# Kernel tuning notes

Hardware: AMD Instinct MI355X
Metric: run time of the kernel (lower is better)

Reference implementation:

```python
import jax, jax.numpy as jnp
import numpy as np

N = 100000      # n_nodes
E = 1600000     # n_edges (avg degree 16)
D_IN, D_H, D_OUT = 128, 64, 16


def setup_inputs() -> dict:
    key = jax.random.key(0)
    k1, k2, k3, k4 = jax.random.split(key, 4)
    x = jax.random.normal(k1, (N, D_IN), dtype=jnp.float32)
    edge_index = jax.random.randint(k2, (2, E), 0, N, dtype=jnp.int32)
    W1 = jax.random.normal(k3, (D_IN, D_H), dtype=jnp.float32) / np.sqrt(D_IN)
    b1 = jnp.zeros((D_H,), dtype=jnp.float32)
    W2 = jax.random.normal(k4, (D_H, D_OUT), dtype=jnp.float32) / np.sqrt(D_H)
    b2 = jnp.zeros((D_OUT,), dtype=jnp.float32)
    return {"x": x, "edge_index": edge_index, "W1": W1, "b1": b1, "W2": W2, "b2": b2}


def gcn_conv(x, src, dst, W, b, n):
    """PyG GCNConv: linear transform, then deg^-1/2 A deg^-1/2 aggregation, + bias.
    src/dst already include self-loops."""
    h = x @ W                                              # [n, d_out]
    deg = jax.ops.segment_sum(jnp.ones_like(dst, dtype=h.dtype), dst, num_segments=n)
    dinv = jnp.where(deg > 0, jax.lax.rsqrt(jnp.maximum(deg, 1.0)), 0.0)
    norm = dinv[src] * dinv[dst]                           # [E+n]
    msgs = h[src] * norm[:, None]                          # gather + scale
    out = jax.ops.segment_sum(msgs, dst, num_segments=n)   # scatter-add
    return out + b


def reference(x, edge_index, W1, b1, W2, b2):
    loops = jnp.arange(N, dtype=edge_index.dtype)
    src = jnp.concatenate([edge_index[0], loops])
    dst = jnp.concatenate([edge_index[1], loops])
    h = jax.nn.relu(gcn_conv(x, src, dst, W1, b1, N))
    return gcn_conv(h, src, dst, W2, b2, N)
```

## Files before the change

kernel.cpp:

```cpp
#include <hip/hip_runtime.h>
#include <cstdint>

#define N_NODES 100000
#define N_EDGES 1600000
#define D_IN    128
#define D_H     64
#define D_OUT   16
#define M_TILES 6250

#define NBKT   512
#define NPB    196
#define BCAP   4096
#define TILE_E 4096
#define NTILES ((N_EDGES + TILE_E - 1) / TILE_E)
#define G1     391
#define GEMM_BLOCKS ((M_TILES + 3) / 4)
#define FUSED_LDS 32768

typedef __attribute__((ext_vector_type(8))) short short8;
typedef __attribute__((ext_vector_type(4))) float floatx4;

static __device__ __forceinline__ unsigned short f2bf(float f) {
    unsigned int u = __float_as_uint(f);
    u = u + 0x7FFFu + ((u >> 16) & 1u);
    return (unsigned short)(u >> 16);
}
static __device__ __forceinline__ float bf2f(unsigned short h) {
    return __uint_as_float(((unsigned int)h) << 16);
}


__global__ __launch_bounds__(512) void zero_small_kernel(int* __restrict__ cursors,
                                                         int* __restrict__ srcs) {
    cursors[threadIdx.x] = 0;
    if (threadIdx.x < 16) srcs[N_EDGES + threadIdx.x] = 0;
}

__global__ __launch_bounds__(256) void fused_bin_gemm1_kernel(
        const int* __restrict__ src, const int* __restrict__ dst,
        int* __restrict__ cursors, int* __restrict__ region,
        const float* __restrict__ x, const float* __restrict__ W1,
        float* __restrict__ h_raw) {
    extern __shared__ char smem[];
    const int t = threadIdx.x;

    if (blockIdx.x < G1) {
        int* hcnt  = (int*)smem;
        int* hbase = (int*)(smem + 2048);
        const int tile = blockIdx.x;
        for (int i = t; i < NBKT; i += 256) hcnt[i] = 0;
        __syncthreads();
        int e0 = tile * TILE_E + t * 16;
        int pk[16], bk[16], rk[16];
        bool full = (e0 + 16 <= N_EDGES);
        if (full) {
            const int4* dp = (const int4*)(dst + e0);
            const int4* sp = (const int4*)(src + e0);
            int dv[16], sv[16];
            #pragma unroll
            for (int q = 0; q < 4; ++q) {
                int4 d4 = dp[q]; int4 s4 = sp[q];
                dv[4*q+0]=d4.x; dv[4*q+1]=d4.y; dv[4*q+2]=d4.z; dv[4*q+3]=d4.w;
                sv[4*q+0]=s4.x; sv[4*q+1]=s4.y; sv[4*q+2]=s4.z; sv[4*q+3]=s4.w;
            }
            #pragma unroll
            for (int k = 0; k < 16; ++k) {
                int d = dv[k];
                int b = d / NPB;
                bk[k] = b;
                pk[k] = ((d - b * NPB) << 17) | sv[k];
                rk[k] = atomicAdd(&hcnt[b], 1);
            }
        }
        __syncthreads();
        for (int i = t; i < NBKT; i += 256) {
            int c = hcnt[i];
            if (c > 0) hbase[i] = atomicAdd(&cursors[i], c);
        }
        __syncthreads();
        if (full) {
            #pragma unroll
            for (int k = 0; k < 16; ++k)
                region[bk[k] * BCAP + hbase[bk[k]] + rk[k]] = pk[k];
        }
        return;
    }

    unsigned short* bhi_lds = (unsigned short*)smem;
    unsigned short* blo_lds = (unsigned short*)(smem + 16384);
    for (int e = t; e < 8192; e += 256) {
        int j    = e & 7;
        int lane = (e >> 3) & 63;
        int pair = e >> 9;
        int kc   = pair >> 2;
        int nt   = pair & 3;
        int k = kc * 32 + (lane >> 4) * 8 + j;
        int n = nt * 16 + (lane & 15);
        float w = W1[k * D_H + n];
        unsigned short hi = f2bf(w);
        float lo = w - bf2f(hi);
        bhi_lds[e] = hi;
        blo_lds[e] = f2bf(lo);
    }
    __syncthreads();

    int wid  = t >> 6;
    int lane = t & 63;
    int quad = lane >> 4;
    int m    = lane & 15;

    int tile = (blockIdx.x - G1) * 4 + wid;
    if (tile >= M_TILES) return;
    int mbase = tile * 16;

    const float* xr = x + (size_t)(mbase + m) * D_IN + quad * 8;
    short8 ahi[4], alo[4];
    #pragma unroll
    for (int kc = 0; kc < 4; ++kc) {
        floatx4 v0 = *(const floatx4*)(xr + kc * 32);
        floatx4 v1 = *(const floatx4*)(xr + kc * 32 + 4);
        float f[8] = {v0.x, v0.y, v0.z, v0.w, v1.x, v1.y, v1.z, v1.w};
        #pragma unroll
        for (int j = 0; j < 8; ++j) {
            unsigned short hi = f2bf(f[j]);
            float lo = f[j] - bf2f(hi);
            ahi[kc][j] = (short)hi;
            alo[kc][j] = (short)f2bf(lo);
        }
    }

    floatx4 acc[4] = {{0.f,0.f,0.f,0.f},{0.f,0.f,0.f,0.f},{0.f,0.f,0.f,0.f},{0.f,0.f,0.f,0.f}};
    #pragma unroll
    for (int kc = 0; kc < 4; ++kc) {
        #pragma unroll
        for (int nt = 0; nt < 4; ++nt) {
            int fo = ((kc * 4 + nt) * 64 + lane) * 8;
            short8 bhi = *(const short8*)&bhi_lds[fo];
            short8 blo = *(const short8*)&blo_lds[fo];
            acc[nt] = __builtin_amdgcn_mfma_f32_16x16x32_bf16(ahi[kc], bhi, acc[nt], 0, 0, 0);
            acc[nt] = __builtin_amdgcn_mfma_f32_16x16x32_bf16(ahi[kc], blo, acc[nt], 0, 0, 0);
            acc[nt] = __builtin_amdgcn_mfma_f32_16x16x32_bf16(alo[kc], bhi, acc[nt], 0, 0, 0);
        }
    }

    #pragma unroll
    for (int nt = 0; nt < 4; ++nt) {
        int col = nt * 16 + m;
        #pragma unroll
        for (int r = 0; r < 4; ++r) {
            int row = mbase + quad * 4 + r;
            h_raw[(size_t)row * D_H + col] = acc[nt][r];
        }
    }
}

__global__ __launch_bounds__(256) void build_kernel(const int* __restrict__ cursors,
                                                    const int* __restrict__ region,
                                                    int* __restrict__ offsets,
                                                    float* __restrict__ dinv,
                                                    int* __restrict__ srcs,
                                                    const float* __restrict__ h_raw,
                                                    unsigned short* __restrict__ hs) {
    __shared__ int lhist[NPB];
    __shared__ int lscan[NPB + 1];
    __shared__ int sbuf[256];
    __shared__ int srt[BCAP];
    __shared__ int red[4];
    __shared__ float sdv[NPB];
    int b = blockIdx.x;
    int t = threadIdx.x;

    int c0 = cursors[t];
    int c1 = cursors[t + 256];
    int p = ((t < b) ? c0 : 0) + ((t + 256 < b) ? c1 : 0);
    int lane = t & 63, wid = t >> 6;
    #pragma unroll
    for (int off = 32; off > 0; off >>= 1) p += __shfl_down(p, off);
    if (lane == 0) red[wid] = p;
    __syncthreads();
    int base = red[0] + red[1] + red[2] + red[3];
    int cnt = cursors[b];
    const int* reg = region + b * BCAP;

    for (int i = t; i < NPB; i += 256) lhist[i] = 0;
    __syncthreads();
    for (int i = t; i < cnt; i += 256) {
        int ln = reg[i] >> 17;
        atomicAdd(&lhist[ln], 1);
    }
    __syncthreads();
    int v = (t < NPB) ? lhist[t] : 0;
    sbuf[t] = v;
    __syncthreads();
    for (int off = 1; off < 256; off <<= 1) {
        int u = (t >= off) ? sbuf[t - off] : 0;
        __syncthreads();
        sbuf[t] += u;
        __syncthreads();
    }
    int incl = sbuf[t];
    if (t < NPB) lscan[t] = incl - v;
    if (t == NPB - 1) lscan[NPB] = incl;
    __syncthreads();
    if (t < NPB) lhist[t] = incl - v;
    __syncthreads();

    int node0 = b * NPB;
    int nlim = N_NODES - node0;
    if (nlim > NPB) nlim = NPB;
    if (t < nlim) {
        offsets[node0 + t] = base + lscan[t];
        int c = lscan[t + 1] - lscan[t];
        float dvv = rsqrtf((float)c + 1.0f);
        dinv[node0 + t] = dvv;
        sdv[t] = dvv;
    }
    if (b == (N_NODES - 1) / NPB && t == 0) offsets[N_NODES] = base + cnt;

    for (int i = t; i < cnt; i += 256) {
        int pk = reg[i];
        int ln = pk >> 17;
        int pos = atomicAdd(&lhist[ln], 1);
        srt[pos] = pk & 0x1FFFF;
    }
    __syncthreads();
    for (int i = t; i < cnt; i += 256) srcs[base + i] = srt[i];

    int tot = nlim * D_H;
    for (int i = t; i < tot; i += 256) {
        int r = i >> 6;
        int c = i & 63;
        size_t off = (size_t)(node0 + r) * D_H + c;
        hs[off] = f2bf(h_raw[off] * sdv[r]);
    }
}

__global__ __launch_bounds__(256) void agg1_fused_kernel(const unsigned short* __restrict__ hs,
                                                         const int* __restrict__ offsets,
                                                         const int* __restrict__ srcs,
                                                         const float* __restrict__ dinv,
                                                         const float* __restrict__ b1,
                                                         const float* __restrict__ W2,
                                                         float* __restrict__ h2s) {
    __shared__ float w2t[16 * 68];
    __shared__ float rbuf[16 * 68];

    const int tid = threadIdx.x;
    for (int i = tid; i < 1024; i += 256) {
        int j = i >> 4, c = i & 15;
        w2t[c * 68 + j] = W2[i];
    }

    const int g    = tid >> 4;
    const int sl   = tid & 15;
    const int node = blockIdx.x * 16 + g;
    const int c4   = sl * 4;

    const int beg = offsets[node];
    const int end = offsets[node + 1];

    ushort4 s4v = *(const ushort4*)(hs + (size_t)node * D_H + c4);
    float a0 = bf2f(s4v.x), a1 = bf2f(s4v.y), a2 = bf2f(s4v.z), a3 = bf2f(s4v.w);

    for (int e = beg; e < end; e += 16) {
        int rem = end - e;
        int idx = srcs[e + sl];
        #pragma unroll
        for (int k = 0; k < 16; ++k) {
            int j = __shfl(idx, k, 16);
            ushort4 v = *(const ushort4*)(hs + (size_t)j * D_H + c4);
            float m = (k < rem) ? 1.0f : 0.0f;
            a0 = fmaf(bf2f(v.x), m, a0);
            a1 = fmaf(bf2f(v.y), m, a1);
            a2 = fmaf(bf2f(v.z), m, a2);
            a3 = fmaf(bf2f(v.w), m, a3);
        }
    }

    const float dv = dinv[node];
    const floatx4 bb = *(const floatx4*)(b1 + c4);
    float* rb = rbuf + g * 68;
    rb[c4 + 0] = fmaxf(a0 * dv + bb.x, 0.f);
    rb[c4 + 1] = fmaxf(a1 * dv + bb.y, 0.f);
    rb[c4 + 2] = fmaxf(a2 * dv + bb.z, 0.f);
    rb[c4 + 3] = fmaxf(a3 * dv + bb.w, 0.f);
    __syncthreads();

    float p = 0.f;
    #pragma unroll
    for (int t4 = 0; t4 < 16; ++t4) {
        floatx4 rv = *(const floatx4*)(rb + 4 * t4);
        floatx4 wv = *(const floatx4*)(&w2t[sl * 68 + 4 * t4]);
        p += rv.x * wv.x + rv.y * wv.y + rv.z * wv.z + rv.w * wv.w;
    }
    h2s[node * D_OUT + sl] = p * dv;
}

__global__ __launch_bounds__(256) void agg2_kernel(const float* __restrict__ h2s,
                                                   const int* __restrict__ offsets,
                                                   const int* __restrict__ srcs,
                                                   const float* __restrict__ dinv,
                                                   const float* __restrict__ b2,
                                                   float* __restrict__ out) {
    int col = threadIdx.x & 15;
    int nidx = (blockIdx.x * blockDim.x + threadIdx.x) >> 4;
    int stride = (gridDim.x * blockDim.x) >> 4;
    for (int node = nidx; node < N_NODES; node += stride) {
        int beg = offsets[node], end = offsets[node + 1];
        float acc = h2s[node * D_OUT + col];
        for (int e = beg; e < end; e += 16) {
            int rem = end - e;
            const int* ep = srcs + e;
            int jj[16];
            #pragma unroll
            for (int k = 0; k < 16; ++k) jj[k] = ep[k];
            float vv[16];
            #pragma unroll
            for (int k = 0; k < 16; ++k) vv[k] = h2s[jj[k] * D_OUT + col];
            #pragma unroll
            for (int k = 0; k < 16; ++k) {
                float m = (k < rem) ? 1.0f : 0.0f;
                acc = fmaf(vv[k], m, acc);
            }
        }
        out[node * D_OUT + col] = acc * dinv[node] + b2[col];
    }
}

extern "C" void kernel_launch(void* const* d_in, const int* in_sizes, int n_in,
                              void* d_out, int out_size, void* d_ws, size_t ws_size,
                              hipStream_t stream) {
    const float* x  = (const float*)d_in[0];
    const int*   ei = (const int*)d_in[1];
    const float* W1 = (const float*)d_in[2];
    const float* b1 = (const float*)d_in[3];
    const float* W2 = (const float*)d_in[4];
    const float* b2 = (const float*)d_in[5];
    float* out = (float*)d_out;

    const int* src = ei;
    const int* dst = ei + N_EDGES;

    char* w = (char*)d_ws;
    int*   cursors  = (int*)(w + 0);
    int*   offsets  = (int*)(w + 4096);
    float* dinv     = (float*)(w + 404224);
    int*   srcs     = (int*)(w + 804224);
    unsigned short* hs = (unsigned short*)(w + 7204352);
    float* h2s      = (float*)(w + 20004480);
    int*   region   = (int*)(w + 26404480);
    float* h_raw    = (float*)(w + 34793088);

    zero_small_kernel<<<1, 512, 0, stream>>>(cursors, srcs);
    fused_bin_gemm1_kernel<<<G1 + GEMM_BLOCKS, 256, FUSED_LDS, stream>>>(
        src, dst, cursors, region, x, W1, h_raw);
    build_kernel<<<NBKT, 256, 0, stream>>>(cursors, region, offsets, dinv, srcs,
                                           h_raw, hs);
    agg1_fused_kernel<<<6250, 256, 0, stream>>>(hs, offsets, srcs, dinv, b1, W2, h2s);
    agg2_kernel<<<6250, 256, 0, stream>>>(h2s, offsets, srcs, dinv, b2, out);
}
```

Before: 199.8 us.

## Interleave binning and GEMM blocks, process two M-tiles per GEMM block

The fused kernel now interleaves blocks: every third block bins an edge tile and the rest run the GEMM, so the two kinds of work are spread across the grid instead of all binning blocks being scheduled first. Each GEMM block now handles 8 row tiles, two per wave, with both tiles' x rows loaded up front. This halves the number of W1 bf16-split LDS preparations and keeps more global loads in flight. The cost is more registers per thread (two sets of x fragments), which may lower occupancy.

```diff
diff --git a/kernel.cpp b/kernel.cpp
--- a/kernel.cpp
+++ b/kernel.cpp
@@ -13,8 +13,8 @@
 #define BCAP   4096
 #define TILE_E 4096
 #define NTILES ((N_EDGES + TILE_E - 1) / TILE_E)
-#define G1     391
-#define GEMM_BLOCKS ((M_TILES + 3) / 4)
+#define GEMM_BLOCKS ((M_TILES + 7) / 8)
+#define FUSED_T (GEMM_BLOCKS + NTILES)
 #define FUSED_LDS 32768
 
 typedef __attribute__((ext_vector_type(8))) short short8;
@@ -42,12 +42,13 @@
         const float* __restrict__ x, const float* __restrict__ W1,
         float* __restrict__ h_raw) {
     extern __shared__ char smem[];
-    const int t = threadIdx.x;
-
-    if (blockIdx.x < G1) {
+    const int t   = threadIdx.x;
+    const int bid = blockIdx.x;
+
+    if (bid % 3 == 0) {
         int* hcnt  = (int*)smem;
         int* hbase = (int*)(smem + 2048);
-        const int tile = blockIdx.x;
+        const int tile = bid / 3;
         for (int i = t; i < NBKT; i += 256) hcnt[i] = 0;
         __syncthreads();
         int e0 = tile * TILE_E + t * 16;
@@ -104,52 +105,79 @@
     }
     __syncthreads();
 
-    int wid  = t >> 6;
-    int lane = t & 63;
-    int quad = lane >> 4;
-    int m    = lane & 15;
-
-    int tile = (blockIdx.x - G1) * 4 + wid;
-    if (tile >= M_TILES) return;
-    int mbase = tile * 16;
-
-    const float* xr = x + (size_t)(mbase + m) * D_IN + quad * 8;
-    short8 ahi[4], alo[4];
+    const int gidx = bid - bid / 3 - 1;
+    const int wid  = t >> 6;
+    const int lane = t & 63;
+    const int quad = lane >> 4;
+    const int m    = lane & 15;
+
+    const int tA = gidx * 8 + wid;
+    const int tB = tA + 4;
+    const bool vA = (tA < M_TILES);
+    const bool vB = (tB < M_TILES);
+
+    floatx4 xA[8], xB[8];
+    if (vA) {
+        const float* xr = x + (size_t)(tA * 16 + m) * D_IN + quad * 8;
+        #pragma unroll
+        for (int kc = 0; kc < 4; ++kc) {
+            xA[2*kc]   = *(const floatx4*)(xr + kc * 32);
+            xA[2*kc+1] = *(const floatx4*)(xr + kc * 32 + 4);
+        }
+    }
+    if (vB) {
+        const float* xr = x + (size_t)(tB * 16 + m) * D_IN + quad * 8;
+        #pragma unroll
+        for (int kc = 0; kc < 4; ++kc) {
+            xB[2*kc]   = *(const floatx4*)(xr + kc * 32);
+            xB[2*kc+1] = *(const floatx4*)(xr + kc * 32 + 4);
+        }
+    }
+
     #pragma unroll
-    for (int kc = 0; kc < 4; ++kc) {
-        floatx4 v0 = *(const floatx4*)(xr + kc * 32);
-        floatx4 v1 = *(const floatx4*)(xr + kc * 32 + 4);
-        float f[8] = {v0.x, v0.y, v0.z, v0.w, v1.x, v1.y, v1.z, v1.w};
-        #pragma unroll
-        for (int j = 0; j < 8; ++j) {
-            unsigned short hi = f2bf(f[j]);
-            float lo = f[j] - bf2f(hi);
-            ahi[kc][j] = (short)hi;
-            alo[kc][j] = (short)f2bf(lo);
-        }
-    }
-
-    floatx4 acc[4] = {{0.f,0.f,0.f,0.f},{0.f,0.f,0.f,0.f},{0.f,0.f,0.f,0.f},{0.f,0.f,0.f,0.f}};
-    #pragma unroll
-    for (int kc = 0; kc < 4; ++kc) {
+    for (int half = 0; half < 2; ++half) {
+        const bool valid = half ? vB : vA;
+        if (!valid) continue;
+        const int tile = half ? tB : tA;
+        const floatx4* xs = half ? xB : xA;
+        const int mbase = tile * 16;
+
+        short8 ahi[4], alo[4];
+        #pragma unroll
+        for (int kc = 0; kc < 4; ++kc) {
+            floatx4 v0 = xs[2*kc], v1 = xs[2*kc+1];
+            float f[8] = {v0.x, v0.y, v0.z, v0.w, v1.x, v1.y, v1.z, v1.w};
+            #pragma unroll
+            for (int j = 0; j < 8; ++j) {
+                unsigned short hi = f2bf(f[j]);
+                float lo = f[j] - bf2f(hi);
+                ahi[kc][j] = (short)hi;
+                alo[kc][j] = (short)f2bf(lo);
+            }
+        }
+
+        floatx4 acc[4] = {{0.f,0.f,0.f,0.f},{0.f,0.f,0.f,0.f},{0.f,0.f,0.f,0.f},{0.f,0.f,0.f,0.f}};
+        #pragma unroll
+        for (int kc = 0; kc < 4; ++kc) {
+            #pragma unroll
+            for (int nt = 0; nt < 4; ++nt) {
+                int fo = ((kc * 4 + nt) * 64 + lane) * 8;
+                short8 bhi = *(const short8*)&bhi_lds[fo];
+                short8 blo = *(const short8*)&blo_lds[fo];
+                acc[nt] = __builtin_amdgcn_mfma_f32_16x16x32_bf16(ahi[kc], bhi, acc[nt], 0, 0, 0);
+                acc[nt] = __builtin_amdgcn_mfma_f32_16x16x32_bf16(ahi[kc], blo, acc[nt], 0, 0, 0);
+                acc[nt] = __builtin_amdgcn_mfma_f32_16x16x32_bf16(alo[kc], bhi, acc[nt], 0, 0, 0);
+            }
+        }
+
         #pragma unroll
         for (int nt = 0; nt < 4; ++nt) {
-            int fo = ((kc * 4 + nt) * 64 + lane) * 8;
-            short8 bhi = *(const short8*)&bhi_lds[fo];
-            short8 blo = *(const short8*)&blo_lds[fo];
-            acc[nt] = __builtin_amdgcn_mfma_f32_16x16x32_bf16(ahi[kc], bhi, acc[nt], 0, 0, 0);
-            acc[nt] = __builtin_amdgcn_mfma_f32_16x16x32_bf16(ahi[kc], blo, acc[nt], 0, 0, 0);
-            acc[nt] = __builtin_amdgcn_mfma_f32_16x16x32_bf16(alo[kc], bhi, acc[nt], 0, 0, 0);
-        }
-    }
-
-    #pragma unroll
-    for (int nt = 0; nt < 4; ++nt) {
-        int col = nt * 16 + m;
-        #pragma unroll
-        for (int r = 0; r < 4; ++r) {
-            int row = mbase + quad * 4 + r;
-            h_raw[(size_t)row * D_H + col] = acc[nt][r];
+            int col = nt * 16 + m;
+            #pragma unroll
+            for (int r = 0; r < 4; ++r) {
+                int row = mbase + quad * 4 + r;
+                h_raw[(size_t)row * D_H + col] = acc[nt][r];
+            }
         }
     }
 }
@@ -352,7 +380,7 @@
     float* h_raw    = (float*)(w + 34793088);
 
     zero_small_kernel<<<1, 512, 0, stream>>>(cursors, srcs);
-    fused_bin_gemm1_kernel<<<G1 + GEMM_BLOCKS, 256, FUSED_LDS, stream>>>(
+    fused_bin_gemm1_kernel<<<FUSED_T, 256, FUSED_LDS, stream>>>(
         src, dst, cursors, region, x, W1, h_raw);
     build_kernel<<<NBKT, 256, 0, stream>>>(cursors, region, offsets, dinv, srcs,
                                            h_raw, hs);
```

Result: faster. 195.8 us (-2.0%).
